# Performance work log

Measured on AMD Instinct MI355X. Metric: run time of the kernel, lower is better.

The kernel has to match this reference:

```python
import jax, jax.numpy as jnp
import numpy as np

DIM = 768
NUM_HEADS = 12
HEAD_DIM = DIM // NUM_HEADS
ALL_HEAD_DIM = HEAD_DIM * NUM_HEADS
SCALE = HEAD_DIM ** -0.5


def setup_inputs() -> dict:
    key = jax.random.key(0)
    k1, k2, k3, k4 = jax.random.split(key, 4)
    B, N = 8, 1024
    x = jax.random.normal(k1, (B, N, DIM), dtype=jnp.float32)
    # qkv_bias=False -> no qkv bias; proj has bias (nn.Linear default)
    w_qkv = jax.random.normal(k2, (DIM, 3 * ALL_HEAD_DIM), dtype=jnp.float32) * (DIM ** -0.5)
    w_proj = jax.random.normal(k3, (ALL_HEAD_DIM, DIM), dtype=jnp.float32) * (ALL_HEAD_DIM ** -0.5)
    b_proj = jax.random.normal(k4, (DIM,), dtype=jnp.float32) * 0.02
    return {"x": x, "w_qkv": w_qkv, "w_proj": w_proj, "b_proj": b_proj}


def reference(x, w_qkv, w_proj, b_proj):
    B, N, C = x.shape
    qkv = (x @ w_qkv).reshape(B, N, 3, NUM_HEADS, HEAD_DIM)
    qkv = jnp.transpose(qkv, (2, 0, 3, 1, 4))  # [3, B, H, N, D]
    q, k, v = qkv[0], qkv[1], qkv[2]
    attn = jax.nn.softmax(jnp.einsum('bhnd,bhmd->bhnm', q * SCALE, k), axis=-1)
    out = jnp.einsum('bhnm,bhmd->bhnd', attn, v)  # [B, H, N, D]
    out = jnp.transpose(out, (0, 2, 1, 3)).reshape(B, N, ALL_HEAD_DIM)
    return out @ w_proj + b_proj
```

## Files before the change

### kernel.cpp

```cpp
#include <hip/hip_runtime.h>

#define NH 12
#define HD 64
#define SEQ 1024
#define BATCH 8
#define DIM 768
#define QKVN 2304
#define ROWS 8192

typedef __bf16 bf16x8 __attribute__((ext_vector_type(8)));
typedef float f32x4 __attribute__((ext_vector_type(4)));
typedef unsigned short u16x8 __attribute__((ext_vector_type(8)));
typedef unsigned short u16x4 __attribute__((ext_vector_type(4)));
typedef short s16x4 __attribute__((ext_vector_type(4)));

__device__ __forceinline__ unsigned short f2bf(float f) {
  union { float f; unsigned int u; } c; c.f = f;
  unsigned int u = c.u;
  u += 0x7fffu + ((u >> 16) & 1u);
  return (unsigned short)(u >> 16);
}

__device__ __forceinline__ void gload_lds16(const unsigned short* g, unsigned short* l) {
  __builtin_amdgcn_global_load_lds(
      (const __attribute__((address_space(1))) void*)g,
      (__attribute__((address_space(3))) void*)l, 16, 0, 0);
}

__global__ void cvt_bf16(const float* __restrict__ src, unsigned short* __restrict__ dst, int n4) {
  int i = blockIdx.x * 256 + threadIdx.x;
  if (i >= n4) return;
  float4 v = ((const float4*)src)[i];
  u16x4 o;
  o.x = f2bf(v.x); o.y = f2bf(v.y); o.z = f2bf(v.z); o.w = f2bf(v.w);
  ((u16x4*)dst)[i] = o;
}

__global__ void transpose_bf16(const float* __restrict__ src, unsigned short* __restrict__ dst,
                               int R, int C) {
  __shared__ float tile[32][33];
  int tx = threadIdx.x & 31, ty = threadIdx.x >> 5;
  int c0 = blockIdx.x * 32, r0 = blockIdx.y * 32;
#pragma unroll
  for (int i = 0; i < 4; ++i)
    tile[ty + i * 8][tx] = src[(size_t)(r0 + ty + i * 8) * C + c0 + tx];
  __syncthreads();
#pragma unroll
  for (int i = 0; i < 4; ++i)
    dst[(size_t)(c0 + ty + i * 8) * R + r0 + tx] = f2bf(tile[tx][ty + i * 8]);
}

template <bool BF16_OUT, bool SCALE_Q>
__global__ __launch_bounds__(256, 4) void gemm128(
    const unsigned short* __restrict__ A, const unsigned short* __restrict__ BT,
    void* __restrict__ Cout, const float* __restrict__ bias,
    int M, int N, int K, int nbx, int nbyXCD) {
  __shared__ unsigned short As[2][128 * 32];
  __shared__ unsigned short Bs[2][128 * 32];
  const int tid = threadIdx.x;
  const int wave = tid >> 6, lane = tid & 63, quad = lane >> 4, l16 = lane & 15;
  const int wm = wave >> 1, wn = wave & 1;
  const int g = blockIdx.x & 7, bi = blockIdx.x >> 3;
  const int by = g * nbyXCD + (bi % nbyXCD);
  const int bx = bi / nbyXCD;
  const int bm = by * 128, bn = bx * 128;

  const int r0 = tid >> 2, kc0 = (tid & 3) * 8;
  const unsigned short* Ag = A + (size_t)(bm + r0) * K + kc0;
  const unsigned short* Bg = BT + (size_t)(bn + r0) * K + kc0;
  unsigned short* AsB = &As[0][0];
  unsigned short* BsB = &Bs[0][0];
  const int wdst = (tid & ~63) * 8;

#define STAGE_G(kt, b) do {                                                   \
    int koff_ = (kt) * 32;                                                    \
    gload_lds16(Ag + koff_,                    AsB + (b) * 4096 + wdst);      \
    gload_lds16(Ag + koff_ + (size_t)64 * K,   AsB + (b) * 4096 + wdst + 2048);\
    gload_lds16(Bg + koff_,                    BsB + (b) * 4096 + wdst);      \
    gload_lds16(Bg + koff_ + (size_t)64 * K,   BsB + (b) * 4096 + wdst + 2048);\
  } while (0)

  f32x4 zero4 = {0.f, 0.f, 0.f, 0.f};
  f32x4 acc[4][4];
#pragma unroll
  for (int i = 0; i < 4; ++i)
#pragma unroll
    for (int j = 0; j < 4; ++j) acc[i][j] = zero4;

  const int nkt = K >> 5;
  STAGE_G(0, 0);
  for (int kt = 0; kt < nkt; ++kt) {
    __syncthreads();
    if (kt + 1 < nkt) STAGE_G(kt + 1, (kt + 1) & 1);
    const unsigned short* Ab = AsB + (kt & 1) * 4096;
    const unsigned short* Bb = BsB + (kt & 1) * 4096;
    bf16x8 af[4], bf[4];
#pragma unroll
    for (int mt = 0; mt < 4; ++mt)
      af[mt] = *(const bf16x8*)&Ab[(wm * 64 + mt * 16 + l16) * 32 + quad * 8];
#pragma unroll
    for (int nt = 0; nt < 4; ++nt)
      bf[nt] = *(const bf16x8*)&Bb[(wn * 64 + nt * 16 + l16) * 32 + quad * 8];
#pragma unroll
    for (int mt = 0; mt < 4; ++mt)
#pragma unroll
      for (int nt = 0; nt < 4; ++nt)
        acc[mt][nt] = __builtin_amdgcn_mfma_f32_16x16x32_bf16(af[mt], bf[nt], acc[mt][nt], 0, 0, 0);
  }
#undef STAGE_G

#pragma unroll
  for (int mt = 0; mt < 4; ++mt)
#pragma unroll
    for (int nt = 0; nt < 4; ++nt) {
      int col = bn + wn * 64 + nt * 16 + l16;
      float bv = BF16_OUT ? 0.f : bias[col];
      float scl = (SCALE_Q && col < DIM) ? 0.125f : 1.0f;
#pragma unroll
      for (int r = 0; r < 4; ++r) {
        int row = bm + wm * 64 + mt * 16 + quad * 4 + r;
        float v = acc[mt][nt][r];
        if (BF16_OUT)
          ((unsigned short*)Cout)[(size_t)row * N + col] = f2bf(v * scl);
        else
          ((float*)Cout)[(size_t)row * N + col] = v + bv;
      }
    }
}

#define VS 76
__global__ __launch_bounds__(512, 6) void attn_kernel(
    const unsigned short* __restrict__ qkv, unsigned short* __restrict__ out) {
  __shared__ unsigned short Ks[2][64 * 64];
  __shared__ unsigned short Vts[2][64 * VS];

  const int tid = threadIdx.x;
  const int wave = tid >> 6, lane = tid & 63, quad = lane >> 4, l16 = lane & 15;
  const int x = blockIdx.x;
  const int qt = (x >> 3) & 7;
  const int bh = (x & 7) + 8 * (x >> 6);
  const int b = bh / NH, h = bh % NH;
  const int qcol = h * HD, kcol = DIM + h * HD, vcol = 2 * DIM + h * HD;
  const int rowQ0 = b * SEQ + qt * 128;
  const int rowKV0 = b * SEQ;

  const int kk_s = tid >> 8, rem_s = tid & 255, n_s = rem_s >> 2, kc_s = rem_s & 3;
  const unsigned short* kgp = qkv + (size_t)(rowKV0 + n_s) * QKVN + kcol + kk_s * 32 + kc_s * 8;
  unsigned short* klp = &Ks[0][0] + (tid & ~63) * 8;
  const int vn = tid & 63, vd0 = (tid >> 6) * 8;
  const unsigned short* vgp = qkv + (size_t)(rowKV0 + vn) * QKVN + vcol + vd0;

  bf16x8 qf[2];
  {
    const unsigned short* qp = qkv + (size_t)(rowQ0 + wave * 16 + l16) * QKVN + qcol + quad * 8;
    qf[0] = *(const bf16x8*)qp;
    qf[1] = *(const bf16x8*)(qp + 32);
  }

  u16x8 vreg = *(const u16x8*)vgp;
  gload_lds16(kgp, klp);
  {
    unsigned short* vb = &Vts[0][0];
#pragma unroll
    for (int e = 0; e < 8; ++e)
      vb[(vd0 + e) * VS + vn] = vreg[e];
  }

  f32x4 zero4 = {0.f, 0.f, 0.f, 0.f};
  f32x4 o[4];
#pragma unroll
  for (int dt = 0; dt < 4; ++dt) o[dt] = zero4;
  float lsum = 0.f;

  for (int jt = 0; jt < 16; ++jt) {
    u16x8 vnext;
    if (jt < 15) vnext = *(const u16x8*)(vgp + (size_t)(jt + 1) * 64 * QKVN);
    __syncthreads();
    if (jt < 15)
      gload_lds16(kgp + (size_t)(jt + 1) * 64 * QKVN, klp + ((jt + 1) & 1) * 4096);

    const unsigned short* Kb = &Ks[jt & 1][0];
    const unsigned short* Vb = &Vts[jt & 1][0];

    f32x4 s[4];
#pragma unroll
    for (int nt = 0; nt < 4; ++nt) s[nt] = zero4;
#pragma unroll
    for (int kk = 0; kk < 2; ++kk)
#pragma unroll
      for (int nt = 0; nt < 4; ++nt) {
        bf16x8 kf = *(const bf16x8*)&Kb[kk * 2048 + (nt * 16 + l16) * 32 + quad * 8];
        s[nt] = __builtin_amdgcn_mfma_f32_16x16x32_bf16(kf, qf[kk], s[nt], 0, 0, 0);
      }

    s16x4 pf[4];
#pragma unroll
    for (int nt = 0; nt < 4; ++nt)
#pragma unroll
      for (int r = 0; r < 4; ++r) {
        float p = __expf(s[nt][r]);
        lsum += p;
        pf[nt][r] = (short)f2bf(p);
      }

#pragma unroll
    for (int nt = 0; nt < 4; ++nt)
#pragma unroll
      for (int dt = 0; dt < 4; ++dt) {
        s16x4 vv = *(const s16x4*)&Vb[(dt * 16 + l16) * VS + nt * 16 + quad * 4];
        o[dt] = __builtin_amdgcn_mfma_f32_16x16x16bf16_1k(pf[nt], vv, o[dt], 0, 0, 0);
      }

    if (jt < 15) {
      unsigned short* vb = &Vts[(jt + 1) & 1][0];
#pragma unroll
      for (int e = 0; e < 8; ++e)
        vb[(vd0 + e) * VS + vn] = vnext[e];
    }
  }

  float l = lsum;
  l += __shfl_xor(l, 16);
  l += __shfl_xor(l, 32);
#pragma unroll
  for (int r = 0; r < 4; ++r) {
    float inv = 1.f / __shfl(l, quad * 4 + r);
    int row = rowQ0 + wave * 16 + quad * 4 + r;
#pragma unroll
    for (int dt = 0; dt < 4; ++dt)
      out[(size_t)row * DIM + h * HD + dt * 16 + l16] = f2bf(o[dt][r] * inv);
  }
}

extern "C" void kernel_launch(void* const* d_in, const int* in_sizes, int n_in,
                              void* d_out, int out_size, void* d_ws, size_t ws_size,
                              hipStream_t stream) {
  const float* x = (const float*)d_in[0];
  const float* w_qkv = (const float*)d_in[1];
  const float* w_proj = (const float*)d_in[2];
  const float* b_proj = (const float*)d_in[3];
  float* outp = (float*)d_out;

  unsigned short* xb = (unsigned short*)d_ws;
  unsigned short* wqkvT = xb + (size_t)ROWS * DIM;
  unsigned short* wprojT = wqkvT + (size_t)QKVN * DIM;
  unsigned short* qkvb = wprojT + (size_t)DIM * DIM;
  unsigned short* attnb = xb;

  cvt_bf16<<<(ROWS * DIM / 4 + 255) / 256, 256, 0, stream>>>(x, xb, ROWS * DIM / 4);
  transpose_bf16<<<dim3(QKVN / 32, DIM / 32), 256, 0, stream>>>(w_qkv, wqkvT, DIM, QKVN);
  transpose_bf16<<<dim3(DIM / 32, DIM / 32), 256, 0, stream>>>(w_proj, wprojT, DIM, DIM);
  gemm128<true, true><<<dim3(1152), 256, 0, stream>>>(xb, wqkvT, qkvb, nullptr, ROWS, QKVN, DIM, 18, 8);
  attn_kernel<<<dim3(8 * 96), 512, 0, stream>>>(qkvb, attnb);
  gemm128<false, false><<<dim3(384), 256, 0, stream>>>(attnb, wprojT, outp, b_proj, ROWS, DIM, DIM, 6, 8);
}
```

Measured before the change: 196.1 us.

## Fuse prep kernels into one launch and shrink GEMM tile to 128x64

```diff
diff --git a/kernel.cpp b/kernel.cpp
--- a/kernel.cpp
+++ b/kernel.cpp
@@ -27,20 +27,10 @@
       (__attribute__((address_space(3))) void*)l, 16, 0, 0);
 }
 
-__global__ void cvt_bf16(const float* __restrict__ src, unsigned short* __restrict__ dst, int n4) {
-  int i = blockIdx.x * 256 + threadIdx.x;
-  if (i >= n4) return;
-  float4 v = ((const float4*)src)[i];
-  u16x4 o;
-  o.x = f2bf(v.x); o.y = f2bf(v.y); o.z = f2bf(v.z); o.w = f2bf(v.w);
-  ((u16x4*)dst)[i] = o;
-}
-
-__global__ void transpose_bf16(const float* __restrict__ src, unsigned short* __restrict__ dst,
-                               int R, int C) {
-  __shared__ float tile[32][33];
+__device__ __forceinline__ void tr_tile(const float* __restrict__ src, unsigned short* __restrict__ dst,
+                                        int R, int C, int bx, int by, float tile[32][33]) {
   int tx = threadIdx.x & 31, ty = threadIdx.x >> 5;
-  int c0 = blockIdx.x * 32, r0 = blockIdx.y * 32;
+  int c0 = bx * 32, r0 = by * 32;
 #pragma unroll
   for (int i = 0; i < 4; ++i)
     tile[ty + i * 8][tx] = src[(size_t)(r0 + ty + i * 8) * C + c0 + tx];
@@ -50,20 +40,39 @@
     dst[(size_t)(c0 + ty + i * 8) * R + r0 + tx] = f2bf(tile[tx][ty + i * 8]);
 }
 
+__global__ void prep_kernel(const float* __restrict__ x, unsigned short* __restrict__ xb,
+                            const float* __restrict__ w_qkv, unsigned short* __restrict__ wqkvT,
+                            const float* __restrict__ w_proj, unsigned short* __restrict__ wprojT) {
+  __shared__ float tile[32][33];
+  int blk = blockIdx.x;
+  if (blk < 6144) {
+    int i = blk * 256 + threadIdx.x;
+    float4 v = ((const float4*)x)[i];
+    u16x4 o;
+    o.x = f2bf(v.x); o.y = f2bf(v.y); o.z = f2bf(v.z); o.w = f2bf(v.w);
+    ((u16x4*)xb)[i] = o;
+  } else if (blk < 6144 + 1728) {
+    int t = blk - 6144;
+    tr_tile(w_qkv, wqkvT, DIM, QKVN, t % 72, t / 72, tile);
+  } else {
+    int t = blk - 6144 - 1728;
+    tr_tile(w_proj, wprojT, DIM, DIM, t % 24, t / 24, tile);
+  }
+}
+
 template <bool BF16_OUT, bool SCALE_Q>
-__global__ __launch_bounds__(256, 4) void gemm128(
+__global__ __launch_bounds__(256, 5) void gemm64(
     const unsigned short* __restrict__ A, const unsigned short* __restrict__ BT,
     void* __restrict__ Cout, const float* __restrict__ bias,
-    int M, int N, int K, int nbx, int nbyXCD) {
+    int M, int N, int K, int nbyXCD) {
   __shared__ unsigned short As[2][128 * 32];
-  __shared__ unsigned short Bs[2][128 * 32];
+  __shared__ unsigned short Bs[2][64 * 32];
   const int tid = threadIdx.x;
   const int wave = tid >> 6, lane = tid & 63, quad = lane >> 4, l16 = lane & 15;
-  const int wm = wave >> 1, wn = wave & 1;
   const int g = blockIdx.x & 7, bi = blockIdx.x >> 3;
   const int by = g * nbyXCD + (bi % nbyXCD);
   const int bx = bi / nbyXCD;
-  const int bm = by * 128, bn = bx * 128;
+  const int bm = by * 128, bn = bx * 64;
 
   const int r0 = tid >> 2, kc0 = (tid & 3) * 8;
   const unsigned short* Ag = A + (size_t)(bm + r0) * K + kc0;
@@ -72,18 +81,17 @@
   unsigned short* BsB = &Bs[0][0];
   const int wdst = (tid & ~63) * 8;
 
-#define STAGE_G(kt, b) do {                                                   \
-    int koff_ = (kt) * 32;                                                    \
-    gload_lds16(Ag + koff_,                    AsB + (b) * 4096 + wdst);      \
-    gload_lds16(Ag + koff_ + (size_t)64 * K,   AsB + (b) * 4096 + wdst + 2048);\
-    gload_lds16(Bg + koff_,                    BsB + (b) * 4096 + wdst);      \
-    gload_lds16(Bg + koff_ + (size_t)64 * K,   BsB + (b) * 4096 + wdst + 2048);\
+#define STAGE_G(kt, b) do {                                                    \
+    int koff_ = (kt) * 32;                                                     \
+    gload_lds16(Ag + koff_,                  AsB + (b) * 4096 + wdst);         \
+    gload_lds16(Ag + koff_ + (size_t)64 * K, AsB + (b) * 4096 + wdst + 2048);  \
+    gload_lds16(Bg + koff_,                  BsB + (b) * 2048 + wdst);         \
   } while (0)
 
   f32x4 zero4 = {0.f, 0.f, 0.f, 0.f};
-  f32x4 acc[4][4];
-#pragma unroll
-  for (int i = 0; i < 4; ++i)
+  f32x4 acc[2][4];
+#pragma unroll
+  for (int i = 0; i < 2; ++i)
 #pragma unroll
     for (int j = 0; j < 4; ++j) acc[i][j] = zero4;
 
@@ -93,16 +101,16 @@
     __syncthreads();
     if (kt + 1 < nkt) STAGE_G(kt + 1, (kt + 1) & 1);
     const unsigned short* Ab = AsB + (kt & 1) * 4096;
-    const unsigned short* Bb = BsB + (kt & 1) * 4096;
-    bf16x8 af[4], bf[4];
-#pragma unroll
-    for (int mt = 0; mt < 4; ++mt)
-      af[mt] = *(const bf16x8*)&Ab[(wm * 64 + mt * 16 + l16) * 32 + quad * 8];
+    const unsigned short* Bb = BsB + (kt & 1) * 2048;
+    bf16x8 af[2], bf[4];
+#pragma unroll
+    for (int mt = 0; mt < 2; ++mt)
+      af[mt] = *(const bf16x8*)&Ab[(wave * 32 + mt * 16 + l16) * 32 + quad * 8];
 #pragma unroll
     for (int nt = 0; nt < 4; ++nt)
-      bf[nt] = *(const bf16x8*)&Bb[(wn * 64 + nt * 16 + l16) * 32 + quad * 8];
-#pragma unroll
-    for (int mt = 0; mt < 4; ++mt)
+      bf[nt] = *(const bf16x8*)&Bb[(nt * 16 + l16) * 32 + quad * 8];
+#pragma unroll
+    for (int mt = 0; mt < 2; ++mt)
 #pragma unroll
       for (int nt = 0; nt < 4; ++nt)
         acc[mt][nt] = __builtin_amdgcn_mfma_f32_16x16x32_bf16(af[mt], bf[nt], acc[mt][nt], 0, 0, 0);
@@ -110,15 +118,15 @@
 #undef STAGE_G
 
 #pragma unroll
-  for (int mt = 0; mt < 4; ++mt)
+  for (int mt = 0; mt < 2; ++mt)
 #pragma unroll
     for (int nt = 0; nt < 4; ++nt) {
-      int col = bn + wn * 64 + nt * 16 + l16;
+      int col = bn + nt * 16 + l16;
       float bv = BF16_OUT ? 0.f : bias[col];
       float scl = (SCALE_Q && col < DIM) ? 0.125f : 1.0f;
 #pragma unroll
       for (int r = 0; r < 4; ++r) {
-        int row = bm + wm * 64 + mt * 16 + quad * 4 + r;
+        int row = bm + wave * 32 + mt * 16 + quad * 4 + r;
         float v = acc[mt][nt][r];
         if (BF16_OUT)
           ((unsigned short*)Cout)[(size_t)row * N + col] = f2bf(v * scl);
@@ -247,10 +255,8 @@
   unsigned short* qkvb = wprojT + (size_t)DIM * DIM;
   unsigned short* attnb = xb;
 
-  cvt_bf16<<<(ROWS * DIM / 4 + 255) / 256, 256, 0, stream>>>(x, xb, ROWS * DIM / 4);
-  transpose_bf16<<<dim3(QKVN / 32, DIM / 32), 256, 0, stream>>>(w_qkv, wqkvT, DIM, QKVN);
-  transpose_bf16<<<dim3(DIM / 32, DIM / 32), 256, 0, stream>>>(w_proj, wprojT, DIM, DIM);
-  gemm128<true, true><<<dim3(1152), 256, 0, stream>>>(xb, wqkvT, qkvb, nullptr, ROWS, QKVN, DIM, 18, 8);
+  prep_kernel<<<dim3(6144 + 1728 + 576), 256, 0, stream>>>(x, xb, w_qkv, wqkvT, w_proj, wprojT);
+  gemm64<true, true><<<dim3(2304), 256, 0, stream>>>(xb, wqkvT, qkvb, nullptr, ROWS, QKVN, DIM, 8);
   attn_kernel<<<dim3(8 * 96), 512, 0, stream>>>(qkvb, attnb);
-  gemm128<false, false><<<dim3(384), 256, 0, stream>>>(attnb, wprojT, outp, b_proj, ROWS, DIM, DIM, 6, 8);
-}
+  gemm64<false, false><<<dim3(768), 256, 0, stream>>>(attnb, wprojT, outp, b_proj, ROWS, DIM, DIM, 8);
+}
```

Result: no change. 192.2 us (-1.9%).
